# Kernel tuning notes

Hardware: AMD Instinct MI355X
Metric: run time of the kernel (lower is better)

The kernel has to match this reference:

```python
import jax, jax.numpy as jnp
import numpy as np
import math

D_MODEL = 1024
N_HEADS = 16
HEAD_DIM = D_MODEL // N_HEADS
B, T = 4, 2048


def setup_inputs() -> dict:
    key = jax.random.key(0)
    k1, k2, k3, k4, k5 = jax.random.split(key, 5)
    s = 1.0 / math.sqrt(D_MODEL)
    return {
        "x": jax.random.normal(k1, (B, T, D_MODEL), dtype=jnp.float32),
        "qkv_w": jax.random.normal(k2, (3 * D_MODEL, D_MODEL), dtype=jnp.float32) * s,
        "qkv_b": jax.random.normal(k3, (3 * D_MODEL,), dtype=jnp.float32) * 0.02,
        "out_w": jax.random.normal(k4, (D_MODEL, D_MODEL), dtype=jnp.float32) * s,
        "out_b": jax.random.normal(k5, (D_MODEL,), dtype=jnp.float32) * 0.02,
    }


def reference(x, qkv_w, qkv_b, out_w, out_b) -> jnp.ndarray:
    b, t, c = x.shape
    h, hd = N_HEADS, HEAD_DIM
    # qkv projection: [B,T,3C]
    qkv = jnp.einsum("btc,oc->bto", x, qkv_w) + qkv_b
    qkv = qkv.reshape(b, t, 3, h, hd).transpose(2, 0, 3, 1, 4)  # [3,B,H,T,hd]
    q, k, v = qkv[0], qkv[1], qkv[2]
    scale = 1.0 / math.sqrt(hd)
    attn = jnp.einsum("bhqd,bhkd->bhqk", q, k) * scale  # [B,H,T,T]
    causal = jnp.triu(jnp.ones((t, t), dtype=bool), k=1)
    attn = jnp.where(causal, -jnp.inf, attn)
    attn = jax.nn.softmax(attn, axis=-1)
    out = jnp.einsum("bhqk,bhkd->bhqd", attn, v)  # [B,H,T,hd]
    out = out.transpose(0, 2, 1, 3).reshape(b, t, c)
    return jnp.einsum("btc,oc->bto", out, out_w) + out_b
```

## Files before the change

### kernel.cpp

```cpp
#include <hip/hip_runtime.h>
#include <stdint.h>
#include <stddef.h>

#define TT 2048
#define NH 16
#define HD 64
#define CM 1024
#define QSCALE 0.1803368801f
#define PPAD 72

typedef float f32x4  __attribute__((ext_vector_type(4)));
typedef short bf16x8 __attribute__((ext_vector_type(8)));

static __device__ __forceinline__ unsigned short f32_to_bf16(float f) {
    union { float f; unsigned u; } c; c.f = f;
    unsigned u = c.u;
    u += 0x7FFFu + ((u >> 16) & 1u);
    return (unsigned short)(u >> 16);
}

static __device__ __forceinline__ unsigned pack_bf16_trunc(float lo, float hi) {
    return __builtin_amdgcn_perm(__float_as_uint(hi), __float_as_uint(lo), 0x07060302u);
}

static __device__ __forceinline__ void glds16(const unsigned short* g, unsigned short* l) {
    __builtin_amdgcn_global_load_lds(
        (const __attribute__((address_space(1))) unsigned int*)g,
        (__attribute__((address_space(3))) unsigned int*)l,
        16, 0, 0);
}

static __device__ __forceinline__ void hard_barrier() {
    asm volatile("s_waitcnt vmcnt(0) lgkmcnt(0)" ::: "memory");
    __syncthreads();
}

__global__ __launch_bounds__(256) void cast_all(
    const float* __restrict__ x, const float* __restrict__ w1,
    const float* __restrict__ w2,
    unsigned short* __restrict__ X16, unsigned short* __restrict__ W1o,
    unsigned short* __restrict__ W2o) {
    int i = blockIdx.x * blockDim.x + threadIdx.x;
    const float* src; unsigned short* dst; int j;
    if (i < 2097152)      { src = x;  dst = X16; j = i; }
    else if (i < 2883584) { src = w1; dst = W1o; j = i - 2097152; }
    else                  { src = w2; dst = W2o; j = i - 2883584; }
    float4 v = ((const float4*)src)[j];
    ushort4 o;
    o.x = f32_to_bf16(v.x); o.y = f32_to_bf16(v.y);
    o.z = f32_to_bf16(v.z); o.w = f32_to_bf16(v.w);
    ((ushort4*)dst)[j] = o;
}

template<bool SWAP>
__device__ __forceinline__ void gemm_core_dbuf(
    const unsigned short* __restrict__ A,
    const unsigned short* __restrict__ Bm,
    int K, int m0, int n0,
    unsigned short* lds,
    f32x4 acc[4][4])
{
    const int tid  = threadIdx.x;
    const int lane = tid & 63;
    const int wm   = ((tid >> 6) >> 1) * 64;
    const int wn   = ((tid >> 6) & 1) * 64;
    const int l15  = lane & 15;
    const int quad = lane >> 4;
    const int rsw  = l15 & 3;

    unsigned short* ldsA = lds;
    unsigned short* ldsB = lds + 8192;

    const int c1 = tid, c2 = tid + 256;
    const int r1 = c1 >> 2, s1 = ((c1 & 3) ^ (r1 & 3)) * 8;
    const int r2 = c2 >> 2, s2 = ((c2 & 3) ^ (r2 & 3)) * 8;
    const unsigned short* gA1 = A  + (size_t)(m0 + r1) * K + s1;
    const unsigned short* gA2 = A  + (size_t)(m0 + r2) * K + s2;
    const unsigned short* gB1 = Bm + (size_t)(n0 + r1) * K + s1;
    const unsigned short* gB2 = Bm + (size_t)(n0 + r2) * K + s2;
    unsigned short* dA1 = ldsA + (c1 & ~63) * 8;
    unsigned short* dA2 = ldsA + (c2 & ~63) * 8;
    unsigned short* dB1 = ldsB + (c1 & ~63) * 8;
    unsigned short* dB2 = ldsB + (c2 & ~63) * 8;

    glds16(gA1, dA1); glds16(gA2, dA2);
    glds16(gB1, dB1); glds16(gB2, dB2);
    gA1 += 32; gA2 += 32; gB1 += 32; gB2 += 32;

    int step = 0;
    for (int k0 = 0; k0 < K; k0 += 32, step ^= 1) {
        hard_barrier();
        if (k0 + 32 < K) {
            const int nx = (step ^ 1) * 4096;
            glds16(gA1, dA1 + nx); glds16(gA2, dA2 + nx);
            glds16(gB1, dB1 + nx); glds16(gB2, dB2 + nx);
            gA1 += 32; gA2 += 32; gB1 += 32; gB2 += 32;
        }
        const unsigned short* tA = ldsA + step * 4096;
        const unsigned short* tB = ldsB + step * 4096;
        const int ro = (quad ^ rsw) * 8;

        bf16x8 af[4], bfr[4];
        #pragma unroll
        for (int mi = 0; mi < 4; ++mi)
            af[mi] = *(const bf16x8*)(tA + (wm + mi * 16 + l15) * 32 + ro);
        #pragma unroll
        for (int ni = 0; ni < 4; ++ni)
            bfr[ni] = *(const bf16x8*)(tB + (wn + ni * 16 + l15) * 32 + ro);

        #pragma unroll
        for (int mi = 0; mi < 4; ++mi)
            #pragma unroll
            for (int ni = 0; ni < 4; ++ni)
                acc[mi][ni] = SWAP
                    ? __builtin_amdgcn_mfma_f32_16x16x32_bf16(bfr[ni], af[mi], acc[mi][ni], 0, 0, 0)
                    : __builtin_amdgcn_mfma_f32_16x16x32_bf16(af[mi], bfr[ni], acc[mi][ni], 0, 0, 0);
    }
}

__global__ __launch_bounds__(256, 2) void gemm_qkv(
    const unsigned short* __restrict__ X,
    const unsigned short* __restrict__ W,
    const float* __restrict__ bias,
    unsigned short* __restrict__ Qb,
    unsigned short* __restrict__ Kb,
    unsigned short* __restrict__ Vt)
{
    __shared__ __align__(16) unsigned short lds[16384];
    const int m0 = blockIdx.y * 128;
    const int n0 = blockIdx.x * 128;

    f32x4 acc[4][4];
    f32x4 z = {0.f, 0.f, 0.f, 0.f};
    #pragma unroll
    for (int mi = 0; mi < 4; ++mi)
        #pragma unroll
        for (int ni = 0; ni < 4; ++ni) acc[mi][ni] = z;

    const bool qk = (n0 < 2048);
    if (qk) gemm_core_dbuf<true >(X, W, CM, m0, n0, lds, acc);
    else    gemm_core_dbuf<false>(X, W, CM, m0, n0, lds, acc);

    const int tid  = threadIdx.x;
    const int lane = tid & 63;
    const int w    = tid >> 6;
    const int wm   = (w >> 1) * 64;
    const int wn   = (w & 1) * 64;
    const int l15  = lane & 15;
    const int quad = lane >> 4;
    const int b_idx = m0 >> 11;
    const int t0 = m0 & 2047;

    if (!qk) {
        hard_barrier();
        #pragma unroll
        for (int half = 0; half < 2; ++half) {
            if ((w & 1) == half) {
                #pragma unroll
                for (int ni = 0; ni < 4; ++ni) {
                    const int orow = ni * 16 + l15;
                    const float bv = bias[n0 + half * 64 + orow];
                    #pragma unroll
                    for (int mi = 0; mi < 4; ++mi) {
                        uint2 pk;
                        pk.x = (unsigned)f32_to_bf16(acc[mi][ni][0] + bv) |
                               ((unsigned)f32_to_bf16(acc[mi][ni][1] + bv) << 16);
                        pk.y = (unsigned)f32_to_bf16(acc[mi][ni][2] + bv) |
                               ((unsigned)f32_to_bf16(acc[mi][ni][3] + bv) << 16);
                        *(uint2*)(lds + orow * 136 + wm + mi * 16 + quad * 4) = pk;
                    }
                }
            }
            hard_barrier();
            {
                const int row = tid >> 2, seg = tid & 3;
                const int o   = n0 + half * 64 + row;
                const int oin = o & 1023;
                const int hh  = oin >> 6, d = oin & 63;
                unsigned short* dst = Vt + ((size_t)((b_idx << 4) + hh) * HD + d) * TT
                                        + t0 + seg * 32;
                const unsigned short* src = lds + row * 136 + seg * 32;
                #pragma unroll
                for (int u = 0; u < 4; ++u)
                    *(uint4*)(dst + u * 8) = *(const uint4*)(src + u * 8);
            }
            hard_barrier();
        }
        return;
    }

    const int region = n0 >> 10;
    unsigned short* dst0 = region ? Kb : Qb;
    const float scl = region ? 1.0f : QSCALE;
    #pragma unroll
    for (int mi = 0; mi < 4; ++mi) {
        const int gm = m0 + wm + mi * 16 + l15;
        const int b  = gm >> 11, t = gm & 2047;
        #pragma unroll
        for (int ni = 0; ni < 4; ++ni) {
            const int o  = n0 + wn + ni * 16 + quad * 4;
            const float4 bv = *(const float4*)(bias + o);
            const int oin = o & 1023;
            const int hh = oin >> 6, d = oin & 63;
            const int bh = (b << 4) + hh;
            const float v0 = (acc[mi][ni][0] + bv.x) * scl;
            const float v1 = (acc[mi][ni][1] + bv.y) * scl;
            const float v2 = (acc[mi][ni][2] + bv.z) * scl;
            const float v3 = (acc[mi][ni][3] + bv.w) * scl;
            uint2 pk;
            pk.x = (unsigned)f32_to_bf16(v0) | ((unsigned)f32_to_bf16(v1) << 16);
            pk.y = (unsigned)f32_to_bf16(v2) | ((unsigned)f32_to_bf16(v3) << 16);
            *(uint2*)(dst0 + (((size_t)(bh * TT + t)) << 6) + d) = pk;
        }
    }
}

__global__ __launch_bounds__(256, 2) void attn_kernel(
    const unsigned short* __restrict__ Qb,
    const unsigned short* __restrict__ Kb,
    const unsigned short* __restrict__ Vt,
    unsigned short* __restrict__ CTX)
{
    __shared__ __align__(16) unsigned short Kl[2][64 * 64];
    __shared__ __align__(16) unsigned short Vl[2][64 * 64];
    __shared__ __align__(16) unsigned short Pl[8][16 * PPAD];

    const int id = blockIdx.x;
    const int qt = 15 - (id >> 6);
    const int bh = id & 63;
    const int b  = bh >> 4, h = bh & 15;
    const int tid  = threadIdx.x;
    const int lane = tid & 63;
    const int w    = tid >> 6;
    const int l15  = lane & 15;
    const int quad = lane >> 4;
    const int sw   = l15 & 7;
    const int bhh  = b * NH + h;

    const unsigned short* Kbase = Kb + (size_t)bhh * TT * HD;
    const unsigned short* Vbase = Vt + (size_t)bhh * HD * TT;
    const f32x4 z = {0.f, 0.f, 0.f, 0.f};

    const int c1 = tid, c2 = tid + 256;
    const int row1 = c1 >> 3, col1 = ((c1 & 7) ^ (row1 & 7)) * 8;
    const int row2 = c2 >> 3, col2 = ((c2 & 7) ^ (row2 & 7)) * 8;
    unsigned short* dK1 = &Kl[0][(c1 & ~63) * 8];
    unsigned short* dK2 = &Kl[0][(c2 & ~63) * 8];
    unsigned short* dV1 = &Vl[0][(c1 & ~63) * 8];
    unsigned short* dV2 = &Vl[0][(c2 & ~63) * 8];

    const int kt_last = 2 * qt + 1;
    const int qb0 = qt * 128;

    const unsigned short* kp1 = Kbase + (size_t)row1 * HD + col1;
    const unsigned short* kp2 = Kbase + (size_t)row2 * HD + col2;
    const unsigned short* vp1 = Vbase + (size_t)row1 * TT + col1;
    const unsigned short* vp2 = Vbase + (size_t)row2 * TT + col2;

    bf16x8 qf[2][2];
    #pragma unroll
    for (int f = 0; f < 2; ++f) {
        const unsigned short* qr =
            Qb + (size_t)(bhh * TT + qb0 + f * 64 + w * 16 + l15) * HD + quad * 8;
        qf[f][0] = *(const bf16x8*)(qr);
        qf[f][1] = *(const bf16x8*)(qr + 32);
    }

    f32x4 o_acc[2][4];
    #pragma unroll
    for (int f = 0; f < 2; ++f)
        #pragma unroll
        for (int di = 0; di < 4; ++di) o_acc[f][di] = z;
    float lrun[2] = {0.f, 0.f};

    glds16(kp1, dK1); glds16(kp2, dK2);
    glds16(vp1, dV1); glds16(vp2, dV2);
    kp1 += 64 * HD; kp2 += 64 * HD; vp1 += 64; vp2 += 64;

    for (int kt = 0; kt <= kt_last; ++kt) {
        const int cur = kt & 1;
        hard_barrier();
        if (kt < kt_last) {
            const int nx = (cur ^ 1) * 4096;
            glds16(kp1, dK1 + nx); glds16(kp2, dK2 + nx);
            glds16(vp1, dV1 + nx); glds16(vp2, dV2 + nx);
            kp1 += 64 * HD; kp2 += 64 * HD; vp1 += 64; vp2 += 64;
        }

        const unsigned short* Kt = Kl[cur];
        const unsigned short* Vtile = Vl[cur];
        const bool f0act = (kt < kt_last);

        f32x4 s0[4], s1[4];
        #pragma unroll
        for (int ni = 0; ni < 4; ++ni) {
            const unsigned short* kr = Kt + (ni * 16 + l15) * 64;
            bf16x8 kf0 = *(const bf16x8*)(kr + ((quad ^ sw) * 8));
            bf16x8 kf1 = *(const bf16x8*)(kr + (((quad + 4) ^ sw) * 8));
            if (f0act) {
                f32x4 a = __builtin_amdgcn_mfma_f32_16x16x32_bf16(kf0, qf[0][0], z, 0, 0, 0);
                s0[ni] = __builtin_amdgcn_mfma_f32_16x16x32_bf16(kf1, qf[0][1], a, 0, 0, 0);
            }
            f32x4 a1 = __builtin_amdgcn_mfma_f32_16x16x32_bf16(kf0, qf[1][0], z, 0, 0, 0);
            s1[ni] = __builtin_amdgcn_mfma_f32_16x16x32_bf16(kf1, qf[1][1], a1, 0, 0, 0);
        }

        const int qloc = w * 16 + l15;
        if (f0act && kt == 2 * qt) {
            #pragma unroll
            for (int ni = 0; ni < 4; ++ni)
                #pragma unroll
                for (int r = 0; r < 4; ++r)
                    if (ni * 16 + quad * 4 + r > qloc) s0[ni][r] = -1e30f;
        }
        if (kt == kt_last) {
            #pragma unroll
            for (int ni = 0; ni < 4; ++ni)
                #pragma unroll
                for (int r = 0; r < 4; ++r)
                    if (ni * 16 + quad * 4 + r > qloc) s1[ni][r] = -1e30f;
        }

        #define SOFTMAX_P(S, F)                                              \
        {                                                                    \
            float acc_l = 0.f;                                               \
            _Pragma("unroll")                                                \
            for (int ni = 0; ni < 4; ++ni)                                   \
                _Pragma("unroll")                                            \
                for (int r = 0; r < 4; ++r) {                                \
                    float p = __builtin_amdgcn_exp2f(S[ni][r]);              \
                    S[ni][r] = p;                                            \
                    acc_l += p;                                              \
                }                                                            \
            lrun[F] += acc_l;                                                \
            unsigned short* pwf = Pl[w * 2 + F];                             \
            _Pragma("unroll")                                                \
            for (int ni = 0; ni < 4; ++ni) {                                 \
                uint2 pk;                                                    \
                pk.x = pack_bf16_trunc(S[ni][0], S[ni][1]);                  \
                pk.y = pack_bf16_trunc(S[ni][2], S[ni][3]);                  \
                *(uint2*)(pwf + l15 * PPAD + ni * 16 + quad * 4) = pk;       \
            }                                                                \
        }

        if (f0act) SOFTMAX_P(s0, 0);
        SOFTMAX_P(s1, 1);
        #undef SOFTMAX_P

        asm volatile("s_waitcnt lgkmcnt(0)" ::: "memory");

        const unsigned short* pw0 = Pl[w * 2 + 0];
        const unsigned short* pw1 = Pl[w * 2 + 1];
        if (f0act) {
            #pragma unroll
            for (int c = 0; c < 2; ++c) {
                bf16x8 pf0 = *(const bf16x8*)(pw0 + l15 * PPAD + c * 32 + quad * 8);
                bf16x8 pf1 = *(const bf16x8*)(pw1 + l15 * PPAD + c * 32 + quad * 8);
                #pragma unroll
                for (int di = 0; di < 4; ++di) {
                    const unsigned short* vr = Vtile + (di * 16 + l15) * 64
                                             + (((c * 4 + quad) ^ sw) * 8);
                    bf16x8 vf = *(const bf16x8*)(vr);
                    o_acc[0][di] = __builtin_amdgcn_mfma_f32_16x16x32_bf16(vf, pf0, o_acc[0][di], 0, 0, 0);
                    o_acc[1][di] = __builtin_amdgcn_mfma_f32_16x16x32_bf16(vf, pf1, o_acc[1][di], 0, 0, 0);
                }
            }
        } else {
            #pragma unroll
            for (int c = 0; c < 2; ++c) {
                bf16x8 pf1 = *(const bf16x8*)(pw1 + l15 * PPAD + c * 32 + quad * 8);
                #pragma unroll
                for (int di = 0; di < 4; ++di) {
                    const unsigned short* vr = Vtile + (di * 16 + l15) * 64
                                             + (((c * 4 + quad) ^ sw) * 8);
                    bf16x8 vf = *(const bf16x8*)(vr);
                    o_acc[1][di] = __builtin_amdgcn_mfma_f32_16x16x32_bf16(vf, pf1, o_acc[1][di], 0, 0, 0);
                }
            }
        }
    }

    #pragma unroll
    for (int f = 0; f < 2; ++f) {
        float lt = lrun[f];
        lt += __shfl_xor(lt, 16);
        lt += __shfl_xor(lt, 32);
        const float inv = 1.0f / lt;
        unsigned short* crow =
            CTX + (size_t)(b * TT + qb0 + f * 64 + w * 16 + l15) * CM + h * HD;
        #pragma unroll
        for (int di = 0; di < 4; ++di) {
            uint2 pk;
            pk.x = (unsigned)f32_to_bf16(o_acc[f][di][0] * inv) |
                   ((unsigned)f32_to_bf16(o_acc[f][di][1] * inv) << 16);
            pk.y = (unsigned)f32_to_bf16(o_acc[f][di][2] * inv) |
                   ((unsigned)f32_to_bf16(o_acc[f][di][3] * inv) << 16);
            *(uint2*)(crow + di * 16 + quad * 4) = pk;
        }
    }
}

__global__ __launch_bounds__(256, 2) void gemm_out(
    const unsigned short* __restrict__ CTX,
    const unsigned short* __restrict__ W,
    const float* __restrict__ bias,
    float* __restrict__ out)
{
    __shared__ __align__(16) unsigned short lds[16384];
    const int m0 = blockIdx.y * 128;
    const int n0 = blockIdx.x * 128;

    f32x4 acc[4][4];
    f32x4 z = {0.f, 0.f, 0.f, 0.f};
    #pragma unroll
    for (int mi = 0; mi < 4; ++mi)
        #pragma unroll
        for (int ni = 0; ni < 4; ++ni) acc[mi][ni] = z;

    gemm_core_dbuf<true>(CTX, W, CM, m0, n0, lds, acc);

    const int tid  = threadIdx.x;
    const int lane = tid & 63;
    const int w    = tid >> 6;
    const int wm   = (w >> 1) * 64;
    const int wn   = (w & 1) * 64;
    const int l15  = lane & 15;
    const int quad = lane >> 4;

    #pragma unroll
    for (int mi = 0; mi < 4; ++mi) {
        const int gm = m0 + wm + mi * 16 + l15;
        float* orow = out + (size_t)gm * CM;
        #pragma unroll
        for (int ni = 0; ni < 4; ++ni) {
            const int o = n0 + wn + ni * 16 + quad * 4;
            const float4 bv = *(const float4*)(bias + o);
            float4 v;
            v.x = acc[mi][ni][0] + bv.x;
            v.y = acc[mi][ni][1] + bv.y;
            v.z = acc[mi][ni][2] + bv.z;
            v.w = acc[mi][ni][3] + bv.w;
            *(float4*)(orow + o) = v;
        }
    }
}

extern "C" void kernel_launch(void* const* d_in, const int* in_sizes, int n_in,
                              void* d_out, int out_size, void* d_ws, size_t ws_size,
                              hipStream_t stream) {
    const float* x     = (const float*)d_in[0];
    const float* qkv_w = (const float*)d_in[1];
    const float* qkv_b = (const float*)d_in[2];
    const float* out_w = (const float*)d_in[3];
    const float* out_b = (const float*)d_in[4];
    float* out = (float*)d_out;

    char* ws = (char*)d_ws;
    unsigned short* X16 = (unsigned short*)(ws + 0);
    unsigned short* W1  = (unsigned short*)(ws + 16777216);
    unsigned short* W2  = (unsigned short*)(ws + 23068672);
    unsigned short* Qb  = (unsigned short*)(ws + 25165824);
    unsigned short* Kb  = (unsigned short*)(ws + 41943040);
    unsigned short* Vt  = (unsigned short*)(ws + 58720256);
    unsigned short* CTX = (unsigned short*)(ws + 75497472);

    cast_all<<<12288, 256, 0, stream>>>(x, qkv_w, out_w, X16, W1, W2);

    gemm_qkv<<<dim3(24, 64), 256, 0, stream>>>(X16, W1, qkv_b, Qb, Kb, Vt);
    attn_kernel<<<1024, 256, 0, stream>>>(Qb, Kb, Vt, CTX);
    gemm_out<<<dim3(8, 64), 256, 0, stream>>>(CTX, W2, out_b, out);
}
```

Measured before the change: 256.5 us.

## Enlarge GEMM tiles to 256x128 with finer-grained vmcnt pipelining

Measured after the change: 256.1 us. Within noise of the previous version (-0.2%).

```diff
diff --git a/kernel.cpp b/kernel.cpp
--- a/kernel.cpp
+++ b/kernel.cpp
@@ -53,69 +53,80 @@
 }
 
 template<bool SWAP>
-__device__ __forceinline__ void gemm_core_dbuf(
+__device__ __forceinline__ void gemm256_core(
     const unsigned short* __restrict__ A,
     const unsigned short* __restrict__ Bm,
-    int K, int m0, int n0,
+    int m0, int n0,
     unsigned short* lds,
-    f32x4 acc[4][4])
+    f32x4 acc[8][4])
 {
     const int tid  = threadIdx.x;
     const int lane = tid & 63;
-    const int wm   = ((tid >> 6) >> 1) * 64;
-    const int wn   = ((tid >> 6) & 1) * 64;
+    const int w    = tid >> 6;
     const int l15  = lane & 15;
     const int quad = lane >> 4;
-    const int rsw  = l15 & 3;
+    const int wm   = (w >> 1) * 128;
+    const int wn   = (w & 1) * 64;
+    const int ro   = (quad ^ (l15 & 3)) * 8;
+
+    const int rr = tid >> 2;
+    const int ch = (tid & 3) ^ (rr & 3);
+    const unsigned short* gA = A  + (size_t)(m0 + rr) * CM + ch * 8;
+    const unsigned short* gB = Bm + (size_t)(n0 + rr) * CM + ch * 8;
+    const int wb = (tid & ~63) * 8;
 
     unsigned short* ldsA = lds;
-    unsigned short* ldsB = lds + 8192;
-
-    const int c1 = tid, c2 = tid + 256;
-    const int r1 = c1 >> 2, s1 = ((c1 & 3) ^ (r1 & 3)) * 8;
-    const int r2 = c2 >> 2, s2 = ((c2 & 3) ^ (r2 & 3)) * 8;
-    const unsigned short* gA1 = A  + (size_t)(m0 + r1) * K + s1;
-    const unsigned short* gA2 = A  + (size_t)(m0 + r2) * K + s2;
-    const unsigned short* gB1 = Bm + (size_t)(n0 + r1) * K + s1;
-    const unsigned short* gB2 = Bm + (size_t)(n0 + r2) * K + s2;
-    unsigned short* dA1 = ldsA + (c1 & ~63) * 8;
-    unsigned short* dA2 = ldsA + (c2 & ~63) * 8;
-    unsigned short* dB1 = ldsB + (c1 & ~63) * 8;
-    unsigned short* dB2 = ldsB + (c2 & ~63) * 8;
-
-    glds16(gA1, dA1); glds16(gA2, dA2);
-    glds16(gB1, dB1); glds16(gB2, dB2);
-    gA1 += 32; gA2 += 32; gB1 += 32; gB2 += 32;
-
-    int step = 0;
-    for (int k0 = 0; k0 < K; k0 += 32, step ^= 1) {
-        hard_barrier();
-        if (k0 + 32 < K) {
-            const int nx = (step ^ 1) * 4096;
-            glds16(gA1, dA1 + nx); glds16(gA2, dA2 + nx);
-            glds16(gB1, dB1 + nx); glds16(gB2, dB2 + nx);
-            gA1 += 32; gA2 += 32; gB1 += 32; gB2 += 32;
-        }
-        const unsigned short* tA = ldsA + step * 4096;
-        const unsigned short* tB = ldsB + step * 4096;
-        const int ro = (quad ^ rsw) * 8;
-
-        bf16x8 af[4], bfr[4];
-        #pragma unroll
-        for (int mi = 0; mi < 4; ++mi)
-            af[mi] = *(const bf16x8*)(tA + (wm + mi * 16 + l15) * 32 + ro);
+    unsigned short* ldsB = lds + 16384;
+
+#define STAGE6(bb)                                                    \
+    {                                                                 \
+        unsigned short* dA = ldsA + (bb) * 8192 + wb;                 \
+        unsigned short* dB = ldsB + (bb) * 4096 + wb;                 \
+        glds16(gA,            dA);                                    \
+        glds16(gA +  64 * CM, dA + 2048);                             \
+        glds16(gA + 128 * CM, dA + 4096);                             \
+        glds16(gA + 192 * CM, dA + 6144);                             \
+        glds16(gB,            dB);                                    \
+        glds16(gB +  64 * CM, dB + 2048);                             \
+        gA += 32; gB += 32;                                           \
+    }
+
+    STAGE6(0);
+    STAGE6(1);
+
+    for (int t = 0; t < 32; ++t) {
+        if (t > 0) {
+            asm volatile("s_waitcnt lgkmcnt(0)" ::: "memory");
+            __builtin_amdgcn_s_barrier();
+            asm volatile("" ::: "memory");
+            if (t + 1 < 32) STAGE6((t + 1) & 1);
+        }
+        if (t + 1 < 32) asm volatile("s_waitcnt vmcnt(6)" ::: "memory");
+        else            asm volatile("s_waitcnt vmcnt(0)" ::: "memory");
+        __builtin_amdgcn_s_barrier();
+        asm volatile("" ::: "memory");
+
+        const unsigned short* tA = ldsA + (t & 1) * 8192;
+        const unsigned short* tB = ldsB + (t & 1) * 4096;
+
+        bf16x8 bfr[4];
         #pragma unroll
         for (int ni = 0; ni < 4; ++ni)
             bfr[ni] = *(const bf16x8*)(tB + (wn + ni * 16 + l15) * 32 + ro);
-
-        #pragma unroll
-        for (int mi = 0; mi < 4; ++mi)
+        bf16x8 af[8];
+        #pragma unroll
+        for (int mi = 0; mi < 8; ++mi)
+            af[mi] = *(const bf16x8*)(tA + (wm + mi * 16 + l15) * 32 + ro);
+
+        #pragma unroll
+        for (int mi = 0; mi < 8; ++mi)
             #pragma unroll
             for (int ni = 0; ni < 4; ++ni)
                 acc[mi][ni] = SWAP
                     ? __builtin_amdgcn_mfma_f32_16x16x32_bf16(bfr[ni], af[mi], acc[mi][ni], 0, 0, 0)
                     : __builtin_amdgcn_mfma_f32_16x16x32_bf16(af[mi], bfr[ni], acc[mi][ni], 0, 0, 0);
     }
+#undef STAGE6
 }
 
 __global__ __launch_bounds__(256, 2) void gemm_qkv(
@@ -126,62 +137,62 @@
     unsigned short* __restrict__ Kb,
     unsigned short* __restrict__ Vt)
 {
-    __shared__ __align__(16) unsigned short lds[16384];
-    const int m0 = blockIdx.y * 128;
+    __shared__ __align__(16) unsigned short lds[24576];
+    const int m0 = blockIdx.y * 256;
     const int n0 = blockIdx.x * 128;
 
-    f32x4 acc[4][4];
+    f32x4 acc[8][4];
     f32x4 z = {0.f, 0.f, 0.f, 0.f};
     #pragma unroll
-    for (int mi = 0; mi < 4; ++mi)
+    for (int mi = 0; mi < 8; ++mi)
         #pragma unroll
         for (int ni = 0; ni < 4; ++ni) acc[mi][ni] = z;
 
-    const bool qk = (n0 < 2048);
-    if (qk) gemm_core_dbuf<true >(X, W, CM, m0, n0, lds, acc);
-    else    gemm_core_dbuf<false>(X, W, CM, m0, n0, lds, acc);
+    const int region = n0 >> 10;
+    if (region < 2) gemm256_core<true >(X, W, m0, n0, lds, acc);
+    else            gemm256_core<false>(X, W, m0, n0, lds, acc);
 
     const int tid  = threadIdx.x;
     const int lane = tid & 63;
     const int w    = tid >> 6;
-    const int wm   = (w >> 1) * 64;
+    const int wm   = (w >> 1) * 128;
     const int wn   = (w & 1) * 64;
     const int l15  = lane & 15;
     const int quad = lane >> 4;
     const int b_idx = m0 >> 11;
     const int t0 = m0 & 2047;
 
-    if (!qk) {
+    if (region == 2) {
         hard_barrier();
         #pragma unroll
-        for (int half = 0; half < 2; ++half) {
-            if ((w & 1) == half) {
+        for (int hn = 0; hn < 2; ++hn) {
+            if ((w & 1) == hn) {
                 #pragma unroll
                 for (int ni = 0; ni < 4; ++ni) {
-                    const int orow = ni * 16 + l15;
-                    const float bv = bias[n0 + half * 64 + orow];
+                    const int nloc = ni * 16 + l15;
+                    const float bv = bias[n0 + hn * 64 + nloc];
                     #pragma unroll
-                    for (int mi = 0; mi < 4; ++mi) {
+                    for (int mi = 0; mi < 8; ++mi) {
                         uint2 pk;
                         pk.x = (unsigned)f32_to_bf16(acc[mi][ni][0] + bv) |
                                ((unsigned)f32_to_bf16(acc[mi][ni][1] + bv) << 16);
                         pk.y = (unsigned)f32_to_bf16(acc[mi][ni][2] + bv) |
                                ((unsigned)f32_to_bf16(acc[mi][ni][3] + bv) << 16);
-                        *(uint2*)(lds + orow * 136 + wm + mi * 16 + quad * 4) = pk;
+                        *(uint2*)(lds + nloc * 264 + wm + mi * 16 + quad * 4) = pk;
                     }
                 }
             }
             hard_barrier();
             {
                 const int row = tid >> 2, seg = tid & 3;
-                const int o   = n0 + half * 64 + row;
+                const int o   = n0 + hn * 64 + row;
                 const int oin = o & 1023;
                 const int hh  = oin >> 6, d = oin & 63;
                 unsigned short* dst = Vt + ((size_t)((b_idx << 4) + hh) * HD + d) * TT
-                                        + t0 + seg * 32;
-                const unsigned short* src = lds + row * 136 + seg * 32;
-                #pragma unroll
-                for (int u = 0; u < 4; ++u)
+                                        + t0 + seg * 64;
+                const unsigned short* src = lds + row * 264 + seg * 64;
+                #pragma unroll
+                for (int u = 0; u < 8; ++u)
                     *(uint4*)(dst + u * 8) = *(const uint4*)(src + u * 8);
             }
             hard_barrier();
@@ -189,20 +200,19 @@
         return;
     }
 
-    const int region = n0 >> 10;
     unsigned short* dst0 = region ? Kb : Qb;
     const float scl = region ? 1.0f : QSCALE;
     #pragma unroll
-    for (int mi = 0; mi < 4; ++mi) {
+    for (int mi = 0; mi < 8; ++mi) {
         const int gm = m0 + wm + mi * 16 + l15;
-        const int b  = gm >> 11, t = gm & 2047;
+        const int t  = gm & 2047;
         #pragma unroll
         for (int ni = 0; ni < 4; ++ni) {
             const int o  = n0 + wn + ni * 16 + quad * 4;
             const float4 bv = *(const float4*)(bias + o);
             const int oin = o & 1023;
             const int hh = oin >> 6, d = oin & 63;
-            const int bh = (b << 4) + hh;
+            const int bh = (b_idx << 4) + hh;
             const float v0 = (acc[mi][ni][0] + bv.x) * scl;
             const float v1 = (acc[mi][ni][1] + bv.y) * scl;
             const float v2 = (acc[mi][ni][2] + bv.z) * scl;
@@ -406,29 +416,29 @@
     const float* __restrict__ bias,
     float* __restrict__ out)
 {
-    __shared__ __align__(16) unsigned short lds[16384];
-    const int m0 = blockIdx.y * 128;
+    __shared__ __align__(16) unsigned short lds[24576];
+    const int m0 = blockIdx.y * 256;
     const int n0 = blockIdx.x * 128;
 
-    f32x4 acc[4][4];
+    f32x4 acc[8][4];
     f32x4 z = {0.f, 0.f, 0.f, 0.f};
     #pragma unroll
-    for (int mi = 0; mi < 4; ++mi)
+    for (int mi = 0; mi < 8; ++mi)
         #pragma unroll
         for (int ni = 0; ni < 4; ++ni) acc[mi][ni] = z;
 
-    gemm_core_dbuf<true>(CTX, W, CM, m0, n0, lds, acc);
+    gemm256_core<true>(CTX, W, m0, n0, lds, acc);
 
     const int tid  = threadIdx.x;
     const int lane = tid & 63;
     const int w    = tid >> 6;
-    const int wm   = (w >> 1) * 64;
+    const int wm   = (w >> 1) * 128;
     const int wn   = (w & 1) * 64;
     const int l15  = lane & 15;
     const int quad = lane >> 4;
 
     #pragma unroll
-    for (int mi = 0; mi < 4; ++mi) {
+    for (int mi = 0; mi < 8; ++mi) {
         const int gm = m0 + wm + mi * 16 + l15;
         float* orow = out + (size_t)gm * CM;
         #pragma unroll
@@ -466,7 +476,7 @@
 
     cast_all<<<12288, 256, 0, stream>>>(x, qkv_w, out_w, X16, W1, W2);
 
-    gemm_qkv<<<dim3(24, 64), 256, 0, stream>>>(X16, W1, qkv_b, Qb, Kb, Vt);
+    gemm_qkv<<<dim3(24, 32), 256, 0, stream>>>(X16, W1, qkv_b, Qb, Kb, Vt);
     attn_kernel<<<1024, 256, 0, stream>>>(Qb, Kb, Vt, CTX);
-    gemm_out<<<dim3(8, 64), 256, 0, stream>>>(CTX, W2, out_b, out);
-}
+    gemm_out<<<dim3(8, 32), 256, 0, stream>>>(CTX, W2, out_b, out);
+}
```
